# Kernel optimization log

Measured on AMD Instinct MI355X. Metric: run time of the kernel, lower is better.

## Reference

```python
import jax, jax.numpy as jnp
import numpy as np

N_NODES = 50000
N_EDGES = 1600000
NUM_MP_STEPS = 6


def _init_linear(key, d_in, d_out):
    kw, kb = jax.random.split(key)
    lim = 1.0 / np.sqrt(d_in)
    W = jax.random.uniform(kw, (d_in, d_out), jnp.float32, -lim, lim)
    b = jax.random.uniform(kb, (d_out,), jnp.float32, -lim, lim)
    return W, b


def setup_inputs() -> dict:
    key = jax.random.key(0)
    ks = jax.random.split(key, 12)
    inp = {
        'x': jax.random.normal(ks[0], (N_NODES, 32), jnp.float32),
        'edge_index': jax.random.randint(ks[1], (2, N_EDGES), 0, N_NODES, jnp.int64),
        'edge_attr': jax.random.normal(ks[2], (N_EDGES, 6), jnp.float32),
    }
    # encoder edge MLP: 6 -> 18 -> 18 -> 16 (leaky relu after every layer)
    inp['enc_W0'], inp['enc_b0'] = _init_linear(ks[3], 6, 18)
    inp['enc_W1'], inp['enc_b1'] = _init_linear(ks[4], 18, 18)
    inp['enc_W2'], inp['enc_b2'] = _init_linear(ks[5], 18, 16)
    # edge model MLP: 160 -> 80 -> 16 (leaky relu)
    inp['edge_W0'], inp['edge_b0'] = _init_linear(ks[6], 160, 80)
    inp['edge_W1'], inp['edge_b1'] = _init_linear(ks[7], 80, 16)
    # node model MLP: 80 -> 56 -> 32 (plain relu: MPGraph does not pass use_leaky_relu here)
    inp['node_W0'], inp['node_b0'] = _init_linear(ks[8], 80, 56)
    inp['node_W1'], inp['node_b1'] = _init_linear(ks[9], 56, 32)
    return inp


def reference(x, edge_index, edge_attr,
              enc_W0, enc_b0, enc_W1, enc_b1, enc_W2, enc_b2,
              edge_W0, edge_b0, edge_W1, edge_b1,
              node_W0, node_b0, node_W1, node_b1):
    lrelu = jax.nn.leaky_relu  # negative_slope=0.01, matches nn.LeakyReLU()
    relu = jax.nn.relu
    row, col = edge_index[0], edge_index[1]
    n_nodes = x.shape[0]

    # encoder on edge feats, LeakyReLU on node feats
    e = lrelu(lrelu(lrelu(edge_attr @ enc_W0 + enc_b0) @ enc_W1 + enc_b1) @ enc_W2 + enc_b2)
    n = lrelu(x)
    e0, n0 = e, n

    ones_e = jnp.ones((row.shape[0], 1), x.dtype)
    outputs = []
    for step in range(1, NUM_MP_STEPS + 1):
        ec = jnp.concatenate([e0, e], axis=1)            # [E, 32] reattach initial edges
        nc = jnp.concatenate([n0, n], axis=1)            # [N, 64] reattach initial nodes
        # edge update: gather endpoints, concat, MLP
        eh = jnp.concatenate([nc[row], nc[col], ec], axis=1)   # [E, 160]
        e = lrelu(lrelu(eh @ edge_W0 + edge_b0) @ edge_W1 + edge_b1)  # [E, 16]
        # node update: scatter-mean messages to source nodes, concat, MLP
        s = jax.ops.segment_sum(e, row, num_segments=n_nodes)         # [N, 16]
        cnt = jax.ops.segment_sum(ones_e, row, num_segments=n_nodes)  # [N, 1]
        msg = s / jnp.maximum(cnt, 1.0)
        nh = jnp.concatenate([nc, msg], axis=1)                        # [N, 80]
        n = relu(relu(nh @ node_W0 + node_b0) @ node_W1 + node_b1)     # [N, 32]
        if step > 1:
            outputs.append(e)
    return tuple(outputs)
```

## Files before the change

### kernel.cpp

```cpp
#include <hip/hip_runtime.h>

#define N_NODES 50000
#define N_EDGES 1600000

#define O_ENCW0 0
#define O_ENCB0 108
#define O_ENCW1 126
#define O_ENCB1 450
#define O_ENCW2 468
#define O_ENCB2 756
#define O_EDGEW0 772
#define O_EDGEB0 13572
#define O_EDGEW1 13652
#define O_EDGEB1 14932
#define O_NODEW0 14948
#define O_NODEB0 19428
#define O_NODEW1 19484
#define O_NODEB1 21276
#define W_TOTAL 21308

typedef __attribute__((ext_vector_type(8))) short bf16x8;
typedef __attribute__((ext_vector_type(4))) short bf16x4;
typedef __attribute__((ext_vector_type(4))) float f32x4;

__device__ __forceinline__ float bf2f(unsigned int u) {
    return __uint_as_float(u << 16);
}
__device__ __forceinline__ unsigned short f2bf(float f) {
    unsigned int u = __float_as_uint(f);
    u += 0x7fffu + ((u >> 16) & 1u);
    return (unsigned short)(u >> 16);
}
__device__ __forceinline__ float lrelu(float x) { return x > 0.f ? x : 0.01f * x; }

__device__ __forceinline__ bf16x8 pack8(float4 a, float4 b) {
    bf16x8 r;
    r[0] = (short)f2bf(a.x); r[1] = (short)f2bf(a.y);
    r[2] = (short)f2bf(a.z); r[3] = (short)f2bf(a.w);
    r[4] = (short)f2bf(b.x); r[5] = (short)f2bf(b.y);
    r[6] = (short)f2bf(b.z); r[7] = (short)f2bf(b.w);
    return r;
}

struct WPack {
    const float* p[14];
    int off[15];
};

__global__ void detect_flags(const int* __restrict__ eidx, int* __restrict__ flags) {
    int t = threadIdx.x;
    int v = eidx[2 * t + 1];
    unsigned long long bi = __ballot(v != 0);
    if (t == 0) flags[0] = (bi == 0ull) ? 1 : 0;
}

__device__ __forceinline__ void load_rc(const int* eidx, int flag64, int e, int& r, int& c) {
    if (flag64) {
        const long long* e64 = (const long long*)eidx;
        r = (int)e64[e];
        c = (int)e64[N_EDGES + e];
    } else {
        r = eidx[e];
        c = eidx[N_EDGES + e];
    }
}
__device__ __forceinline__ int load_r(const int* eidx, int flag64, int e) {
    return flag64 ? (int)((const long long*)eidx)[e] : eidx[e];
}

__global__ void copy_w(WPack P, float* __restrict__ dst) {
    int a = blockIdx.x;
    const float* s = P.p[a];
    int n = P.off[a + 1] - P.off[a];
    float* d = dst + P.off[a];
    for (int i = threadIdx.x; i < n; i += 256) d[i] = s[i];
}

__global__ void build_wT(const float* __restrict__ w0,
                         const float* __restrict__ w1,
                         unsigned short* __restrict__ wT) {
    int t = blockIdx.x * 256 + threadIdx.x;
    if (t < 12800) {
        int col = t / 160, k = t % 160;
        wT[t] = f2bf(w0[k * 80 + col]);
    } else if (t < 14336) {
        int u = t - 12800;
        int col = u / 96, k = u % 96;
        wT[t] = (k < 80) ? f2bf(w1[k * 16 + col]) : (unsigned short)0;
    }
}

__global__ void __launch_bounds__(256) init_nodes(const float* __restrict__ x,
                                                  unsigned short* __restrict__ ncb,
                                                  int* __restrict__ cnti) {
    int i = blockIdx.x * 256 + threadIdx.x;
    if (i >= N_NODES) return;
    const float4* xin = (const float4*)(x + (size_t)i * 32);
    uint4* np = (uint4*)(ncb + (size_t)i * 64);
#pragma unroll
    for (int q = 0; q < 4; q++) {
        float4 a = xin[2 * q];
        float4 b = xin[2 * q + 1];
        unsigned int w0 = (unsigned int)f2bf(lrelu(a.x)) | ((unsigned int)f2bf(lrelu(a.y)) << 16);
        unsigned int w1 = (unsigned int)f2bf(lrelu(a.z)) | ((unsigned int)f2bf(lrelu(a.w)) << 16);
        unsigned int w2 = (unsigned int)f2bf(lrelu(b.x)) | ((unsigned int)f2bf(lrelu(b.y)) << 16);
        unsigned int w3 = (unsigned int)f2bf(lrelu(b.z)) | ((unsigned int)f2bf(lrelu(b.w)) << 16);
        uint4 o = make_uint4(w0, w1, w2, w3);
        np[q] = o;
        np[4 + q] = o;
    }
    cnti[i] = 0;
}

__global__ void count_edges(const int* __restrict__ eidx, const int* __restrict__ flags,
                            int* __restrict__ cnti) {
    int e = blockIdx.x * 256 + threadIdx.x;
    atomicAdd(&cnti[load_r(eidx, flags[0], e)], 1);
}

__global__ void __launch_bounds__(256) scan_offsets(const int* __restrict__ cnti,
                                                    int* __restrict__ off,
                                                    int* __restrict__ cursor) {
    __shared__ int ls[256];
    const int t = threadIdx.x;
    const int lo = t * 196;
    const int hi = min(lo + 196, N_NODES);
    int sum = 0;
    for (int i = lo; i < hi; i++) sum += cnti[i];
    ls[t] = sum;
    __syncthreads();
    for (int d = 1; d < 256; d <<= 1) {
        int v = (t >= d) ? ls[t - d] : 0;
        __syncthreads();
        ls[t] += v;
        __syncthreads();
    }
    int run = (t == 0) ? 0 : ls[t - 1];
    for (int i = lo; i < hi; i++) {
        off[i] = run;
        cursor[i] = run;
        run += cnti[i];
    }
    if (t == 255) off[N_NODES] = run;
}

__global__ void build_perm(const int* __restrict__ eidx, const int* __restrict__ flags,
                           int* __restrict__ cursor, int* __restrict__ perm) {
    int e = blockIdx.x * 256 + threadIdx.x;
    int pos = atomicAdd(&cursor[load_r(eidx, flags[0], e)], 1);
    perm[pos] = e;
}

template <int B16H>
__global__ void __launch_bounds__(256) encoder(const float* __restrict__ ea,
                                               const float* __restrict__ wsW,
                                               float* __restrict__ outbase,
                                               unsigned short* __restrict__ e0b) {
    int e = blockIdx.x * 256 + threadIdx.x;
    const float* ap = ea + (size_t)e * 6;
    float a[6];
#pragma unroll
    for (int k = 0; k < 6; k++) a[k] = ap[k];

    float h1[18];
#pragma unroll
    for (int j = 0; j < 18; j++) h1[j] = wsW[O_ENCB0 + j];
#pragma unroll
    for (int k = 0; k < 6; k++) {
        float v = a[k];
#pragma unroll
        for (int j = 0; j < 18; j++) h1[j] = fmaf(v, wsW[O_ENCW0 + k * 18 + j], h1[j]);
    }
#pragma unroll
    for (int j = 0; j < 18; j++) h1[j] = lrelu(h1[j]);

    float h2[18];
#pragma unroll
    for (int j = 0; j < 18; j++) h2[j] = wsW[O_ENCB1 + j];
#pragma unroll
    for (int k = 0; k < 18; k++) {
        float v = h1[k];
#pragma unroll
        for (int j = 0; j < 18; j++) h2[j] = fmaf(v, wsW[O_ENCW1 + k * 18 + j], h2[j]);
    }
#pragma unroll
    for (int j = 0; j < 18; j++) h2[j] = lrelu(h2[j]);

    float o[16];
#pragma unroll
    for (int j = 0; j < 16; j++) o[j] = wsW[O_ENCB2 + j];
#pragma unroll
    for (int k = 0; k < 18; k++) {
        float v = h2[k];
#pragma unroll
        for (int j = 0; j < 16; j++) o[j] = fmaf(v, wsW[O_ENCW2 + k * 16 + j], o[j]);
    }
    if (B16H) {
        unsigned int pw[8];
#pragma unroll
        for (int q = 0; q < 8; q++) {
            float a0 = lrelu(o[2 * q]), a1 = lrelu(o[2 * q + 1]);
            pw[q] = (unsigned int)f2bf(a0) | ((unsigned int)f2bf(a1) << 16);
        }
        uint4* ow = (uint4*)(e0b + (size_t)e * 16);
        ow[0] = make_uint4(pw[0], pw[1], pw[2], pw[3]);
        ow[1] = make_uint4(pw[4], pw[5], pw[6], pw[7]);
    } else {
        float4* ow = (float4*)(outbase + (size_t)4 * N_EDGES * 16 + (size_t)e * 16);
#pragma unroll
        for (int q = 0; q < 4; q++)
            ow[q] = make_float4(lrelu(o[4 * q]), lrelu(o[4 * q + 1]),
                                lrelu(o[4 * q + 2]), lrelu(o[4 * q + 3]));
    }
}

__global__ void __launch_bounds__(256) edge_mfma(const unsigned short* __restrict__ ncb,
                                                 const float* __restrict__ outb_c,
                                                 int slot_e0, int slot_prev, int slot_cur,
                                                 const int* __restrict__ eidx,
                                                 const int* __restrict__ flags,
                                                 const float* __restrict__ wsW,
                                                 const unsigned short* __restrict__ wT,
                                                 float* __restrict__ outb) {
    __shared__ unsigned short act1[4][32 * 104];
    const int lane = threadIdx.x & 63;
    const int wave = threadIdx.x >> 6;
    const int r16 = lane & 15;
    const int g = lane >> 4;
    const int flag64 = flags[0];
    unsigned short* aw = act1[wave];

    const int ebase = blockIdx.x * 128 + wave * 32;
    const float* e0s = outb_c + (size_t)slot_e0 * N_EDGES * 16;
    const float* eps = outb_c + (size_t)slot_prev * N_EDGES * 16;

#pragma unroll
    for (int u = 0; u < 2; u++) {
        bf16x4 z4 = {0, 0, 0, 0};
        *(bf16x4*)&aw[(u * 16 + r16) * 104 + 80 + g * 4] = z4;
    }

    bf16x8 a[2][5];
#pragma unroll
    for (int u = 0; u < 2; u++) {
        const int el = ebase + u * 16 + r16;
        int r_el, c_el;
        load_rc(eidx, flag64, el, r_el, c_el);
        a[u][0] = *(const bf16x8*)(ncb + (size_t)r_el * 64 + g * 8);
        a[u][1] = *(const bf16x8*)(ncb + (size_t)r_el * 64 + 32 + g * 8);
        a[u][2] = *(const bf16x8*)(ncb + (size_t)c_el * 64 + g * 8);
        a[u][3] = *(const bf16x8*)(ncb + (size_t)c_el * 64 + 32 + g * 8);
        const float* src = (g < 2) ? e0s : eps;
        const float4* p = (const float4*)(src + (size_t)el * 16 + (g & 1) * 8);
        a[u][4] = pack8(p[0], p[1]);
    }

#pragma unroll
    for (int t = 0; t < 5; t++) {
        float bv = wsW[O_EDGEB0 + t * 16 + r16];
        f32x4 acc0 = {bv, bv, bv, bv};
        f32x4 acc1 = {bv, bv, bv, bv};
#pragma unroll
        for (int st = 0; st < 5; st++) {
            bf16x8 b = *(const bf16x8*)(wT + (t * 16 + r16) * 160 + st * 32 + g * 8);
            acc0 = __builtin_amdgcn_mfma_f32_16x16x32_bf16(a[0][st], b, acc0, 0, 0, 0);
            acc1 = __builtin_amdgcn_mfma_f32_16x16x32_bf16(a[1][st], b, acc1, 0, 0, 0);
        }
#pragma unroll
        for (int i = 0; i < 4; i++) {
            aw[(g * 4 + i) * 104 + t * 16 + r16]        = f2bf(lrelu(acc0[i]));
            aw[(16 + g * 4 + i) * 104 + t * 16 + r16]   = f2bf(lrelu(acc1[i]));
        }
    }
    asm volatile("s_waitcnt lgkmcnt(0)" ::: "memory");
    __builtin_amdgcn_sched_barrier(0);

    float bv2 = wsW[O_EDGEB1 + r16];
    f32x4 acc20 = {bv2, bv2, bv2, bv2};
    f32x4 acc21 = {bv2, bv2, bv2, bv2};
#pragma unroll
    for (int st = 0; st < 3; st++) {
        bf16x8 b2 = *(const bf16x8*)(wT + 12800 + r16 * 96 + st * 32 + g * 8);
        bf16x8 a20 = *(const bf16x8*)&aw[r16 * 104 + st * 32 + g * 8];
        bf16x8 a21 = *(const bf16x8*)&aw[(16 + r16) * 104 + st * 32 + g * 8];
        acc20 = __builtin_amdgcn_mfma_f32_16x16x32_bf16(a20, b2, acc20, 0, 0, 0);
        acc21 = __builtin_amdgcn_mfma_f32_16x16x32_bf16(a21, b2, acc21, 0, 0, 0);
    }

    float* oc = outb + (size_t)slot_cur * N_EDGES * 16;
#pragma unroll
    for (int i = 0; i < 4; i++) {
        int eg0 = ebase + g * 4 + i;
        int eg1 = ebase + 16 + g * 4 + i;
        oc[(size_t)eg0 * 16 + r16] = lrelu(acc20[i]);
        oc[(size_t)eg1 * 16 + r16] = lrelu(acc21[i]);
    }
}

template <int WOUT>
__global__ void __launch_bounds__(256) edge_mfma_b16(const unsigned short* __restrict__ ncb,
                                                     const unsigned short* __restrict__ e0b,
                                                     const unsigned short* __restrict__ prevb,
                                                     unsigned short* __restrict__ curb,
                                                     const int* __restrict__ eidx,
                                                     const int* __restrict__ flags,
                                                     const float* __restrict__ wsW,
                                                     const unsigned short* __restrict__ wT,
                                                     float* __restrict__ oc) {
    __shared__ unsigned short act1[4][32 * 104];
    const int lane = threadIdx.x & 63;
    const int wave = threadIdx.x >> 6;
    const int r16 = lane & 15;
    const int g = lane >> 4;
    const int flag64 = flags[0];
    unsigned short* aw = act1[wave];

    const int ebase = blockIdx.x * 128 + wave * 32;

#pragma unroll
    for (int u = 0; u < 2; u++) {
        bf16x4 z4 = {0, 0, 0, 0};
        *(bf16x4*)&aw[(u * 16 + r16) * 104 + 80 + g * 4] = z4;
    }

    bf16x8 a[2][5];
#pragma unroll
    for (int u = 0; u < 2; u++) {
        const int el = ebase + u * 16 + r16;
        int r_el, c_el;
        load_rc(eidx, flag64, el, r_el, c_el);
        a[u][0] = *(const bf16x8*)(ncb + (size_t)r_el * 64 + g * 8);
        a[u][1] = *(const bf16x8*)(ncb + (size_t)r_el * 64 + 32 + g * 8);
        a[u][2] = *(const bf16x8*)(ncb + (size_t)c_el * 64 + g * 8);
        a[u][3] = *(const bf16x8*)(ncb + (size_t)c_el * 64 + 32 + g * 8);
        const unsigned short* src = (g < 2) ? e0b : prevb;
        a[u][4] = *(const bf16x8*)(src + (size_t)el * 16 + (g & 1) * 8);
    }

#pragma unroll
    for (int t = 0; t < 5; t++) {
        float bv = wsW[O_EDGEB0 + t * 16 + r16];
        f32x4 acc0 = {bv, bv, bv, bv};
        f32x4 acc1 = {bv, bv, bv, bv};
#pragma unroll
        for (int st = 0; st < 5; st++) {
            bf16x8 b = *(const bf16x8*)(wT + (t * 16 + r16) * 160 + st * 32 + g * 8);
            acc0 = __builtin_amdgcn_mfma_f32_16x16x32_bf16(a[0][st], b, acc0, 0, 0, 0);
            acc1 = __builtin_amdgcn_mfma_f32_16x16x32_bf16(a[1][st], b, acc1, 0, 0, 0);
        }
#pragma unroll
        for (int i = 0; i < 4; i++) {
            aw[(g * 4 + i) * 104 + t * 16 + r16]        = f2bf(lrelu(acc0[i]));
            aw[(16 + g * 4 + i) * 104 + t * 16 + r16]   = f2bf(lrelu(acc1[i]));
        }
    }
    asm volatile("s_waitcnt lgkmcnt(0)" ::: "memory");
    __builtin_amdgcn_sched_barrier(0);

    float bv2 = wsW[O_EDGEB1 + r16];
    f32x4 acc20 = {bv2, bv2, bv2, bv2};
    f32x4 acc21 = {bv2, bv2, bv2, bv2};
#pragma unroll
    for (int st = 0; st < 3; st++) {
        bf16x8 b2 = *(const bf16x8*)(wT + 12800 + r16 * 96 + st * 32 + g * 8);
        bf16x8 a20 = *(const bf16x8*)&aw[r16 * 104 + st * 32 + g * 8];
        bf16x8 a21 = *(const bf16x8*)&aw[(16 + r16) * 104 + st * 32 + g * 8];
        acc20 = __builtin_amdgcn_mfma_f32_16x16x32_bf16(a20, b2, acc20, 0, 0, 0);
        acc21 = __builtin_amdgcn_mfma_f32_16x16x32_bf16(a21, b2, acc21, 0, 0, 0);
    }

#pragma unroll
    for (int i = 0; i < 4; i++) {
        int eg0 = ebase + g * 4 + i;
        int eg1 = ebase + 16 + g * 4 + i;
        float v0 = lrelu(acc20[i]);
        float v1 = lrelu(acc21[i]);
        curb[(size_t)eg0 * 16 + r16] = f2bf(v0);
        curb[(size_t)eg1 * 16 + r16] = f2bf(v1);
        if (WOUT) {
            oc[(size_t)eg0 * 16 + r16] = v0;
            oc[(size_t)eg1 * 16 + r16] = v1;
        }
    }
}

__global__ void __launch_bounds__(256) gather_mean(const int* __restrict__ off,
                                                   const int* __restrict__ perm,
                                                   const float* __restrict__ ecur,
                                                   float* __restrict__ msg) {
    const int wave = threadIdx.x >> 6;
    const int lane = threadIdx.x & 63;
    const int i = blockIdx.x * 4 + wave;
    const int c = lane & 15;
    const int sub = lane >> 4;
    const int p0 = off[i], p1 = off[i + 1];
    float sum = 0.f;
    for (int p = p0 + sub; p < p1; p += 4)
        sum += ecur[(size_t)perm[p] * 16 + c];
    sum += __shfl_xor(sum, 16, 64);
    sum += __shfl_xor(sum, 32, 64);
    if (lane < 16) {
        float inv = 1.0f / fmaxf((float)(p1 - p0), 1.0f);
        msg[(size_t)i * 16 + c] = sum * inv;
    }
}

__global__ void __launch_bounds__(256) gather_mean_b16(const int* __restrict__ off,
                                                       const int* __restrict__ perm,
                                                       const unsigned short* __restrict__ ecurb,
                                                       float* __restrict__ msg) {
    const int wave = threadIdx.x >> 6;
    const int lane = threadIdx.x & 63;
    const int i = blockIdx.x * 4 + wave;
    const int c = lane & 15;
    const int sub = lane >> 4;
    const int p0 = off[i], p1 = off[i + 1];
    float sum = 0.f;
    for (int p = p0 + sub; p < p1; p += 4)
        sum += bf2f((unsigned int)ecurb[(size_t)perm[p] * 16 + c]);
    sum += __shfl_xor(sum, 16, 64);
    sum += __shfl_xor(sum, 32, 64);
    if (lane < 16) {
        float inv = 1.0f / fmaxf((float)(p1 - p0), 1.0f);
        msg[(size_t)i * 16 + c] = sum * inv;
    }
}

__global__ void __launch_bounds__(64) node_mlp(const float* __restrict__ msg,
                                               unsigned short* __restrict__ ncb,
                                               const float* __restrict__ wsW) {
    __shared__ float sl[64 * 81];
    const int l = threadIdx.x;
    const int i = blockIdx.x * 64 + l;
    if (i >= N_NODES) return;
    const float* W0 = wsW + O_NODEW0;
    const float* b0 = wsW + O_NODEB0;
    const float* W1 = wsW + O_NODEW1;
    const float* b1 = wsW + O_NODEB1;

    const uint4* ncp = (const uint4*)(ncb + (size_t)i * 64);
#pragma unroll
    for (int q = 0; q < 8; q++) {
        uint4 u = ncp[q];
        int base = l * 81 + 8 * q;
        sl[base + 0] = bf2f(u.x & 0xffffu); sl[base + 1] = bf2f(u.x >> 16);
        sl[base + 2] = bf2f(u.y & 0xffffu); sl[base + 3] = bf2f(u.y >> 16);
        sl[base + 4] = bf2f(u.z & 0xffffu); sl[base + 5] = bf2f(u.z >> 16);
        sl[base + 6] = bf2f(u.w & 0xffffu); sl[base + 7] = bf2f(u.w >> 16);
    }
    const float4* mp = (const float4*)(msg + (size_t)i * 16);
#pragma unroll
    for (int q = 0; q < 4; q++) {
        float4 v = mp[q];
        int base = l * 81 + 64 + 4 * q;
        sl[base] = v.x; sl[base + 1] = v.y; sl[base + 2] = v.z; sl[base + 3] = v.w;
    }

    float h[56];
#pragma unroll
    for (int q = 0; q < 14; q++) {
        float4 b = ((const float4*)b0)[q];
        h[4 * q] = b.x; h[4 * q + 1] = b.y; h[4 * q + 2] = b.z; h[4 * q + 3] = b.w;
    }
    for (int k = 0; k < 80; k++) {
        float v = sl[l * 81 + k];
        const float4* w = (const float4*)(W0 + k * 56);
#pragma unroll
        for (int q = 0; q < 14; q++) {
            float4 wv = w[q];
            h[4 * q]     = fmaf(v, wv.x, h[4 * q]);
            h[4 * q + 1] = fmaf(v, wv.y, h[4 * q + 1]);
            h[4 * q + 2] = fmaf(v, wv.z, h[4 * q + 2]);
            h[4 * q + 3] = fmaf(v, wv.w, h[4 * q + 3]);
        }
    }
#pragma unroll
    for (int j = 0; j < 56; j++) sl[l * 81 + j] = fmaxf(h[j], 0.f);

    float o[32];
#pragma unroll
    for (int q = 0; q < 8; q++) {
        float4 b = ((const float4*)b1)[q];
        o[4 * q] = b.x; o[4 * q + 1] = b.y; o[4 * q + 2] = b.z; o[4 * q + 3] = b.w;
    }
    for (int j = 0; j < 56; j++) {
        float v = sl[l * 81 + j];
        const float4* w = (const float4*)(W1 + j * 32);
#pragma unroll
        for (int q = 0; q < 8; q++) {
            float4 wv = w[q];
            o[4 * q]     = fmaf(v, wv.x, o[4 * q]);
            o[4 * q + 1] = fmaf(v, wv.y, o[4 * q + 1]);
            o[4 * q + 2] = fmaf(v, wv.z, o[4 * q + 2]);
            o[4 * q + 3] = fmaf(v, wv.w, o[4 * q + 3]);
        }
    }
    uint4* nout = (uint4*)(ncb + (size_t)i * 64 + 32);
#pragma unroll
    for (int q = 0; q < 4; q++) {
        unsigned int w0 = (unsigned int)f2bf(fmaxf(o[8 * q + 0], 0.f)) |
                          ((unsigned int)f2bf(fmaxf(o[8 * q + 1], 0.f)) << 16);
        unsigned int w1 = (unsigned int)f2bf(fmaxf(o[8 * q + 2], 0.f)) |
                          ((unsigned int)f2bf(fmaxf(o[8 * q + 3], 0.f)) << 16);
        unsigned int w2 = (unsigned int)f2bf(fmaxf(o[8 * q + 4], 0.f)) |
                          ((unsigned int)f2bf(fmaxf(o[8 * q + 5], 0.f)) << 16);
        unsigned int w3 = (unsigned int)f2bf(fmaxf(o[8 * q + 6], 0.f)) |
                          ((unsigned int)f2bf(fmaxf(o[8 * q + 7], 0.f)) << 16);
        nout[q] = make_uint4(w0, w1, w2, w3);
    }
}

extern "C" void kernel_launch(void* const* d_in, const int* in_sizes, int n_in,
                              void* d_out, int out_size, void* d_ws, size_t ws_size,
                              hipStream_t stream) {
    (void)in_sizes; (void)n_in; (void)out_size;
    const float* x  = (const float*)d_in[0];
    const int* eidx = (const int*)d_in[1];
    const float* ea = (const float*)d_in[2];
    float* out = (float*)d_out;

    char* wsb = (char*)d_ws;
    float* wsW  = (float*)(wsb + 0);
    int* flags  = (int*)(wsb + 85232);
    int* cnti   = (int*)(wsb + 85248);
    int* off    = (int*)(wsb + 285248);
    int* cursor = (int*)(wsb + 485264);
    int* perm   = (int*)(wsb + 685264);
    unsigned short* ncb = (unsigned short*)(wsb + 7085264);
    unsigned short* wT  = (unsigned short*)(wsb + 13485264);
    float* msg  = (float*)(wsb + 13513936);
    const size_t WS_BASE = 16713936ull;
    unsigned short* e0b = (unsigned short*)(wsb + 16714240);
    unsigned short* rb0 = e0b + (size_t)N_EDGES * 16;
    unsigned short* rb1 = rb0 + (size_t)N_EDGES * 16;
    const size_t WS_BIG = 16714240ull + 3ull * 51200000ull;
    if (ws_size < WS_BASE) return;
    const bool big = (ws_size >= WS_BIG);

    WPack P;
    static const int offs[15] = {0, 108, 126, 450, 468, 756, 772, 13572, 13652,
                                 14932, 14948, 19428, 19484, 21276, 21308};
    for (int a = 0; a < 14; a++) P.p[a] = (const float*)d_in[3 + a];
    for (int a = 0; a < 15; a++) P.off[a] = offs[a];

    detect_flags<<<1, 64, 0, stream>>>(eidx, flags);
    copy_w<<<14, 256, 0, stream>>>(P, wsW);
    build_wT<<<56, 256, 0, stream>>>((const float*)d_in[9], (const float*)d_in[11], wT);
    init_nodes<<<196, 256, 0, stream>>>(x, ncb, cnti);
    count_edges<<<N_EDGES / 256, 256, 0, stream>>>(eidx, flags, cnti);
    scan_offsets<<<1, 256, 0, stream>>>(cnti, off, cursor);
    build_perm<<<N_EDGES / 256, 256, 0, stream>>>(eidx, flags, cursor, perm);

    if (big) {
        encoder<1><<<N_EDGES / 256, 256, 0, stream>>>(ea, wsW, out, e0b);
        unsigned short* rings[2] = {rb0, rb1};
        for (int t = 1; t <= 6; t++) {
            unsigned short* prevb = (t == 1) ? e0b : rings[(t - 1) & 1];
            unsigned short* curb  = rings[t & 1];
            if (t == 1)
                edge_mfma_b16<0><<<N_EDGES / 128, 256, 0, stream>>>(
                    ncb, e0b, prevb, curb, eidx, flags, wsW, wT, out);
            else
                edge_mfma_b16<1><<<N_EDGES / 128, 256, 0, stream>>>(
                    ncb, e0b, prevb, curb, eidx, flags, wsW, wT,
                    out + (size_t)(t - 2) * N_EDGES * 16);
            if (t < 6) {
                gather_mean_b16<<<12500, 256, 0, stream>>>(off, perm, curb, msg);
                node_mlp<<<782, 64, 0, stream>>>(msg, ncb, wsW);
            }
        }
    } else {
        encoder<0><<<N_EDGES / 256, 256, 0, stream>>>(ea, wsW, out, nullptr);
        const int prevs[6] = {4, 0, 0, 1, 2, 3};
        const int curs[6]  = {0, 0, 1, 2, 3, 4};
        for (int t = 1; t <= 6; t++) {
            edge_mfma<<<N_EDGES / 128, 256, 0, stream>>>(ncb, out, 4, prevs[t - 1],
                                                         curs[t - 1], eidx, flags, wsW,
                                                         wT, out);
            if (t < 6) {
                gather_mean<<<12500, 256, 0, stream>>>(
                    off, perm, out + (size_t)curs[t - 1] * N_EDGES * 16, msg);
                node_mlp<<<782, 64, 0, stream>>>(msg, ncb, wsW);
            }
        }
    }
}
```

Before: 1.764 ms.

## Store edge state in row-sorted order to make scatter-mean reads sequential

Adds a new path, used when the workspace is large enough, that keeps the edge feature buffers in CSR (row-sorted) order. build_perm also records the (row, col) pair per sorted position and each edge's sorted position. The encoder scatters e0 into sorted order, and the edge kernel walks sorted positions. The segment mean can then read contiguous ranges instead of gathering through perm. The cost is that the fp32 outputs are now scattered through perm, and the path needs extra workspace plus more indexing work during setup.

Result: faster. 1.604 ms (-9.1%).

```diff
diff --git a/kernel.cpp b/kernel.cpp
--- a/kernel.cpp
+++ b/kernel.cpp
@@ -144,18 +144,27 @@
     if (t == 255) off[N_NODES] = run;
 }
 
+template <int EXT>
 __global__ void build_perm(const int* __restrict__ eidx, const int* __restrict__ flags,
-                           int* __restrict__ cursor, int* __restrict__ perm) {
+                           int* __restrict__ cursor, int* __restrict__ perm,
+                           int2* __restrict__ rcp, int* __restrict__ pose) {
     int e = blockIdx.x * 256 + threadIdx.x;
-    int pos = atomicAdd(&cursor[load_r(eidx, flags[0], e)], 1);
+    int r, c;
+    load_rc(eidx, flags[0], e, r, c);
+    int pos = atomicAdd(&cursor[r], 1);
     perm[pos] = e;
-}
-
-template <int B16H>
+    if (EXT) {
+        rcp[pos] = make_int2(r, c);
+        pose[e] = pos;
+    }
+}
+
+template <int MODE>
 __global__ void __launch_bounds__(256) encoder(const float* __restrict__ ea,
                                                const float* __restrict__ wsW,
                                                float* __restrict__ outbase,
-                                               unsigned short* __restrict__ e0b) {
+                                               unsigned short* __restrict__ e0b,
+                                               const int* __restrict__ pose) {
     int e = blockIdx.x * 256 + threadIdx.x;
     const float* ap = ea + (size_t)e * 6;
     float a[6];
@@ -195,24 +204,26 @@
 #pragma unroll
         for (int j = 0; j < 16; j++) o[j] = fmaf(v, wsW[O_ENCW2 + k * 16 + j], o[j]);
     }
-    if (B16H) {
+    if (MODE == 0) {
+        float4* ow = (float4*)(outbase + (size_t)4 * N_EDGES * 16 + (size_t)e * 16);
+#pragma unroll
+        for (int q = 0; q < 4; q++)
+            ow[q] = make_float4(lrelu(o[4 * q]), lrelu(o[4 * q + 1]),
+                                lrelu(o[4 * q + 2]), lrelu(o[4 * q + 3]));
+    } else {
         unsigned int pw[8];
 #pragma unroll
         for (int q = 0; q < 8; q++) {
             float a0 = lrelu(o[2 * q]), a1 = lrelu(o[2 * q + 1]);
             pw[q] = (unsigned int)f2bf(a0) | ((unsigned int)f2bf(a1) << 16);
         }
-        uint4* ow = (uint4*)(e0b + (size_t)e * 16);
+        size_t pos = (MODE == 2) ? (size_t)pose[e] : (size_t)e;
+        uint4* ow = (uint4*)(e0b + pos * 16);
         ow[0] = make_uint4(pw[0], pw[1], pw[2], pw[3]);
         ow[1] = make_uint4(pw[4], pw[5], pw[6], pw[7]);
-    } else {
-        float4* ow = (float4*)(outbase + (size_t)4 * N_EDGES * 16 + (size_t)e * 16);
-#pragma unroll
-        for (int q = 0; q < 4; q++)
-            ow[q] = make_float4(lrelu(o[4 * q]), lrelu(o[4 * q + 1]),
-                                lrelu(o[4 * q + 2]), lrelu(o[4 * q + 3]));
-    }
-}
+    }
+}
+
 
 __global__ void __launch_bounds__(256) edge_mfma(const unsigned short* __restrict__ ncb,
                                                  const float* __restrict__ outb_c,
@@ -268,8 +279,8 @@
         }
 #pragma unroll
         for (int i = 0; i < 4; i++) {
-            aw[(g * 4 + i) * 104 + t * 16 + r16]        = f2bf(lrelu(acc0[i]));
-            aw[(16 + g * 4 + i) * 104 + t * 16 + r16]   = f2bf(lrelu(acc1[i]));
+            aw[(g * 4 + i) * 104 + t * 16 + r16]      = f2bf(lrelu(acc0[i]));
+            aw[(16 + g * 4 + i) * 104 + t * 16 + r16] = f2bf(lrelu(acc1[i]));
         }
     }
     asm volatile("s_waitcnt lgkmcnt(0)" ::: "memory");
@@ -350,8 +361,8 @@
         }
 #pragma unroll
         for (int i = 0; i < 4; i++) {
-            aw[(g * 4 + i) * 104 + t * 16 + r16]        = f2bf(lrelu(acc0[i]));
-            aw[(16 + g * 4 + i) * 104 + t * 16 + r16]   = f2bf(lrelu(acc1[i]));
+            aw[(g * 4 + i) * 104 + t * 16 + r16]      = f2bf(lrelu(acc0[i]));
+            aw[(16 + g * 4 + i) * 104 + t * 16 + r16] = f2bf(lrelu(acc1[i]));
         }
     }
     asm volatile("s_waitcnt lgkmcnt(0)" ::: "memory");
@@ -380,6 +391,93 @@
         if (WOUT) {
             oc[(size_t)eg0 * 16 + r16] = v0;
             oc[(size_t)eg1 * 16 + r16] = v1;
+        }
+    }
+}
+
+template <int WOUT>
+__global__ void __launch_bounds__(256) edge_mfma_perm(const unsigned short* __restrict__ ncb,
+                                                      const unsigned short* __restrict__ e0b,
+                                                      const unsigned short* __restrict__ prevb,
+                                                      unsigned short* __restrict__ curb,
+                                                      const int2* __restrict__ rcp,
+                                                      const int* __restrict__ perm,
+                                                      const float* __restrict__ wsW,
+                                                      const unsigned short* __restrict__ wT,
+                                                      float* __restrict__ oc) {
+    __shared__ unsigned short act1[4][32 * 104];
+    const int lane = threadIdx.x & 63;
+    const int wave = threadIdx.x >> 6;
+    const int r16 = lane & 15;
+    const int g = lane >> 4;
+    unsigned short* aw = act1[wave];
+
+    const int pbase = blockIdx.x * 128 + wave * 32;
+
+#pragma unroll
+    for (int u = 0; u < 2; u++) {
+        bf16x4 z4 = {0, 0, 0, 0};
+        *(bf16x4*)&aw[(u * 16 + r16) * 104 + 80 + g * 4] = z4;
+    }
+
+    bf16x8 a[2][5];
+#pragma unroll
+    for (int u = 0; u < 2; u++) {
+        const int pl = pbase + u * 16 + r16;
+        int2 rc = rcp[pl];
+        a[u][0] = *(const bf16x8*)(ncb + (size_t)rc.x * 64 + g * 8);
+        a[u][1] = *(const bf16x8*)(ncb + (size_t)rc.x * 64 + 32 + g * 8);
+        a[u][2] = *(const bf16x8*)(ncb + (size_t)rc.y * 64 + g * 8);
+        a[u][3] = *(const bf16x8*)(ncb + (size_t)rc.y * 64 + 32 + g * 8);
+        const unsigned short* src = (g < 2) ? e0b : prevb;
+        a[u][4] = *(const bf16x8*)(src + (size_t)pl * 16 + (g & 1) * 8);
+    }
+
+#pragma unroll
+    for (int t = 0; t < 5; t++) {
+        float bv = wsW[O_EDGEB0 + t * 16 + r16];
+        f32x4 acc0 = {bv, bv, bv, bv};
+        f32x4 acc1 = {bv, bv, bv, bv};
+#pragma unroll
+        for (int st = 0; st < 5; st++) {
+            bf16x8 b = *(const bf16x8*)(wT + (t * 16 + r16) * 160 + st * 32 + g * 8);
+            acc0 = __builtin_amdgcn_mfma_f32_16x16x32_bf16(a[0][st], b, acc0, 0, 0, 0);
+            acc1 = __builtin_amdgcn_mfma_f32_16x16x32_bf16(a[1][st], b, acc1, 0, 0, 0);
+        }
+#pragma unroll
+        for (int i = 0; i < 4; i++) {
+            aw[(g * 4 + i) * 104 + t * 16 + r16]      = f2bf(lrelu(acc0[i]));
+            aw[(16 + g * 4 + i) * 104 + t * 16 + r16] = f2bf(lrelu(acc1[i]));
+        }
+    }
+    asm volatile("s_waitcnt lgkmcnt(0)" ::: "memory");
+    __builtin_amdgcn_sched_barrier(0);
+
+    float bv2 = wsW[O_EDGEB1 + r16];
+    f32x4 acc20 = {bv2, bv2, bv2, bv2};
+    f32x4 acc21 = {bv2, bv2, bv2, bv2};
+#pragma unroll
+    for (int st = 0; st < 3; st++) {
+        bf16x8 b2 = *(const bf16x8*)(wT + 12800 + r16 * 96 + st * 32 + g * 8);
+        bf16x8 a20 = *(const bf16x8*)&aw[r16 * 104 + st * 32 + g * 8];
+        bf16x8 a21 = *(const bf16x8*)&aw[(16 + r16) * 104 + st * 32 + g * 8];
+        acc20 = __builtin_amdgcn_mfma_f32_16x16x32_bf16(a20, b2, acc20, 0, 0, 0);
+        acc21 = __builtin_amdgcn_mfma_f32_16x16x32_bf16(a21, b2, acc21, 0, 0, 0);
+    }
+
+#pragma unroll
+    for (int i = 0; i < 4; i++) {
+        int p0l = pbase + g * 4 + i;
+        int p1l = pbase + 16 + g * 4 + i;
+        float v0 = lrelu(acc20[i]);
+        float v1 = lrelu(acc21[i]);
+        curb[(size_t)p0l * 16 + r16] = f2bf(v0);
+        curb[(size_t)p1l * 16 + r16] = f2bf(v1);
+        if (WOUT) {
+            int eo0 = perm[p0l];
+            int eo1 = perm[p1l];
+            oc[(size_t)eo0 * 16 + r16] = v0;
+            oc[(size_t)eo1 * 16 + r16] = v1;
         }
     }
 }
@@ -426,6 +524,26 @@
     }
 }
 
+__global__ void __launch_bounds__(256) gather_mean_seq(const int* __restrict__ off,
+                                                       const unsigned short* __restrict__ ecurb,
+                                                       float* __restrict__ msg) {
+    const int wave = threadIdx.x >> 6;
+    const int lane = threadIdx.x & 63;
+    const int i = blockIdx.x * 4 + wave;
+    const int c = lane & 15;
+    const int sub = lane >> 4;
+    const int p0 = off[i], p1 = off[i + 1];
+    float sum = 0.f;
+    for (int p = p0 + sub; p < p1; p += 4)
+        sum += bf2f((unsigned int)ecurb[(size_t)p * 16 + c]);
+    sum += __shfl_xor(sum, 16, 64);
+    sum += __shfl_xor(sum, 32, 64);
+    if (lane < 16) {
+        float inv = 1.0f / fmaxf((float)(p1 - p0), 1.0f);
+        msg[(size_t)i * 16 + c] = sum * inv;
+    }
+}
+
 __global__ void __launch_bounds__(64) node_mlp(const float* __restrict__ msg,
                                                unsigned short* __restrict__ ncb,
                                                const float* __restrict__ wsW) {
@@ -534,8 +652,12 @@
     unsigned short* rb0 = e0b + (size_t)N_EDGES * 16;
     unsigned short* rb1 = rb0 + (size_t)N_EDGES * 16;
     const size_t WS_BIG = 16714240ull + 3ull * 51200000ull;
+    int2* rcp = (int2*)(wsb + 170314240ull);
+    int* pose = (int*)(wsb + 183114240ull);
+    const size_t WS_PERM = 189514240ull;
     if (ws_size < WS_BASE) return;
-    const bool big = (ws_size >= WS_BIG);
+    const bool big  = (ws_size >= WS_BIG);
+    const bool prm  = (ws_size >= WS_PERM);
 
     WPack P;
     static const int offs[15] = {0, 108, 126, 450, 468, 756, 772, 13572, 13652,
@@ -549,10 +671,31 @@
     init_nodes<<<196, 256, 0, stream>>>(x, ncb, cnti);
     count_edges<<<N_EDGES / 256, 256, 0, stream>>>(eidx, flags, cnti);
     scan_offsets<<<1, 256, 0, stream>>>(cnti, off, cursor);
-    build_perm<<<N_EDGES / 256, 256, 0, stream>>>(eidx, flags, cursor, perm);
-
-    if (big) {
-        encoder<1><<<N_EDGES / 256, 256, 0, stream>>>(ea, wsW, out, e0b);
+    if (prm)
+        build_perm<1><<<N_EDGES / 256, 256, 0, stream>>>(eidx, flags, cursor, perm, rcp, pose);
+    else
+        build_perm<0><<<N_EDGES / 256, 256, 0, stream>>>(eidx, flags, cursor, perm, nullptr, nullptr);
+
+    if (prm) {
+        encoder<2><<<N_EDGES / 256, 256, 0, stream>>>(ea, wsW, out, e0b, pose);
+        unsigned short* rings[2] = {rb0, rb1};
+        for (int t = 1; t <= 6; t++) {
+            unsigned short* prevb = (t == 1) ? e0b : rings[(t - 1) & 1];
+            unsigned short* curb  = rings[t & 1];
+            if (t == 1)
+                edge_mfma_perm<0><<<N_EDGES / 128, 256, 0, stream>>>(
+                    ncb, e0b, prevb, curb, rcp, perm, wsW, wT, out);
+            else
+                edge_mfma_perm<1><<<N_EDGES / 128, 256, 0, stream>>>(
+                    ncb, e0b, prevb, curb, rcp, perm, wsW, wT,
+                    out + (size_t)(t - 2) * N_EDGES * 16);
+            if (t < 6) {
+                gather_mean_seq<<<12500, 256, 0, stream>>>(off, curb, msg);
+                node_mlp<<<782, 64, 0, stream>>>(msg, ncb, wsW);
+            }
+        }
+    } else if (big) {
+        encoder<1><<<N_EDGES / 256, 256, 0, stream>>>(ea, wsW, out, e0b, nullptr);
         unsigned short* rings[2] = {rb0, rb1};
         for (int t = 1; t <= 6; t++) {
             unsigned short* prevb = (t == 1) ? e0b : rings[(t - 1) & 1];
@@ -570,7 +713,7 @@
             }
         }
     } else {
-        encoder<0><<<N_EDGES / 256, 256, 0, stream>>>(ea, wsW, out, nullptr);
+        encoder<0><<<N_EDGES / 256, 256, 0, stream>>>(ea, wsW, out, nullptr, nullptr);
         const int prevs[6] = {4, 0, 0, 1, 2, 3};
         const int curs[6]  = {0, 0, 1, 2, 3, 4};
         for (int t = 1; t <= 6; t++) {
```
